# Performance work log

Measured on AMD Instinct MI355X. Metric: run time of the kernel, lower is better.

## Reference

```python
import jax, jax.numpy as jnp
import numpy as np

B, T, H, IN, OUT = 128, 256, 1024, 1, 1


def setup_inputs() -> dict:
    key = jax.random.key(0)
    ks = jax.random.split(key, 11)
    s = 1.0 / np.sqrt(H)
    u = lambda k, shape: jax.random.uniform(k, shape, jnp.float32, -s, s)
    return {
        "input_X": jax.random.normal(ks[0], (B, T), jnp.float32),
        "W_ih0": u(ks[1], (4 * H, IN)),
        "W_hh0": u(ks[2], (4 * H, H)),
        "b_ih0": u(ks[3], (4 * H,)),
        "b_hh0": u(ks[4], (4 * H,)),
        "W_ih1": u(ks[5], (4 * H, H)),
        "W_hh1": u(ks[6], (4 * H, H)),
        "b_ih1": u(ks[7], (4 * H,)),
        "b_hh1": u(ks[8], (4 * H,)),
        "W_lin": u(ks[9], (OUT, H)),
        "b_lin": u(ks[10], (OUT,)),
        "future": 0,
    }


def _lstm_cell(x, h, c, W_ih, W_hh, b_ih, b_hh):
    # gates: [B, 4H], PyTorch LSTMCell gate order: i, f, g, o
    gates = x @ W_ih.T + b_ih + h @ W_hh.T + b_hh
    i, f, g, o = jnp.split(gates, 4, axis=-1)
    c_new = jax.nn.sigmoid(f) * c + jax.nn.sigmoid(i) * jnp.tanh(g)
    h_new = jax.nn.sigmoid(o) * jnp.tanh(c_new)
    return h_new, c_new


def reference(input_X, W_ih0, W_hh0, b_ih0, b_hh0, W_ih1, W_hh1, b_ih1, b_hh1,
              W_lin, b_lin, future):
    batch = input_X.shape[0]
    h0 = jnp.zeros((batch, H), input_X.dtype)
    c0 = jnp.zeros((batch, H), input_X.dtype)
    h1 = jnp.zeros((batch, H), input_X.dtype)
    c1 = jnp.zeros((batch, H), input_X.dtype)

    def step(carry, x_t):  # x_t: [B, 1]
        h0, c0, h1, c1 = carry
        h0, c0 = _lstm_cell(x_t, h0, c0, W_ih0, W_hh0, b_ih0, b_hh0)
        h1, c1 = _lstm_cell(h0, h1, c1, W_ih1, W_hh1, b_ih1, b_hh1)
        y = h1 @ W_lin.T + b_lin  # [B, OUT]
        return (h0, c0, h1, c1), y

    xs = input_X.T[:, :, None]  # [T, B, 1]
    carry, ys = jax.lax.scan(step, (h0, c0, h1, c1), xs)
    outputs = jnp.transpose(ys, (1, 0, 2))  # [B, T, OUT]

    y = ys[-1]
    fut = []
    for _ in range(int(future)):
        carry, y = step(carry, y)
        fut.append(y)
    if fut:
        outputs = jnp.concatenate([outputs, jnp.stack(fut, axis=1)], axis=1)
    return jnp.squeeze(outputs, axis=2)  # [B, T+future]
```

## Files before the change

kernel.cpp:

```cpp
#include <hip/hip_runtime.h>
#include <stdint.h>

typedef _Float16 f16;
typedef f16 half8 __attribute__((ext_vector_type(8)));
typedef float f32x4 __attribute__((ext_vector_type(4)));

#define AS1 __attribute__((address_space(1)))
#define AS3 __attribute__((address_space(3)))

constexpr int HID = 1024;
constexpr int NBAT = 128;
constexpr int SEQ = 256;
constexpr int NL0 = 64;
constexpr int NL1 = 128;
constexpr int NBLK = NL0 + NL1;
constexpr int HROWB = 4096;
constexpr int WROWB0 = 2064;
constexpr int WROWB1 = 4112;
constexpr int ZOFF = 32 * WROWB1;
constexpr int ZBYTES = 4160;
constexpr int WLDS = ZOFF + ZBYTES;
constexpr int CHB = 8192;
constexpr int LDS_TOTAL = WLDS + 3 * CHB;

constexpr int SY_INIT = 0;
constexpr int SY_BARG = 32;
constexpr int SY_CNT = 64;
constexpr int SY_BARAX = 64 + 256;
constexpr int SY_TOTAL = 64 + 256 + 256;

__device__ __forceinline__ float sigm(float x) { return 1.0f / (1.0f + __expf(-x)); }
__device__ __forceinline__ float tanh_(float x) {
  float e = __expf(2.0f * x);
  return (e - 1.0f) / (e + 1.0f);
}
__device__ __forceinline__ void gl_lds16(const void* g, void* l) {
  __builtin_amdgcn_global_load_lds((const AS1 uint32_t*)g, (AS3 uint32_t*)l, 16, 0, 0);
}
__device__ __forceinline__ void vm0() {
  asm volatile("s_waitcnt vmcnt(0)" ::: "memory");
}
__device__ __forceinline__ void spin_until(int* p, int target) {
  uint64_t t0 = __builtin_amdgcn_s_memtime();
  while (__hip_atomic_load(p, __ATOMIC_RELAXED, __HIP_MEMORY_SCOPE_AGENT) < target) {
    __builtin_amdgcn_s_sleep(1);
    if (__builtin_amdgcn_s_memtime() - t0 > (1ULL << 29)) break;
  }
}

__global__ __launch_bounds__(256, 1) void lstm_persist(
    const float* __restrict__ X,
    const float* __restrict__ Wih0, const float* __restrict__ Whh0,
    const float* __restrict__ bih0, const float* __restrict__ bhh0,
    const float* __restrict__ Wih1, const float* __restrict__ Whh1,
    const float* __restrict__ bih1, const float* __restrict__ bhh1,
    const float* __restrict__ Wlin,
    f16* __restrict__ Hcat,
    float* __restrict__ yp,
    int* __restrict__ sy) {
  extern __shared__ char smem[];
  char* Wl = smem;
  char* Ach = smem + WLDS;

  const int bid = blockIdx.x, tid = threadIdx.x;
  const bool isL0 = bid < NL0;
  const int j = isL0 ? bid : bid - NL0;
  const int w = tid >> 6, l = tid & 63;
  const int l15 = l & 15, lhi = l >> 4;

  int xcd;
  asm volatile("s_getreg_b32 %0, hwreg(HW_REG_XCC_ID)" : "=s"(xcd));
  xcd &= 7;

  if (isL0) {
    for (int it = 0; it < 256; ++it) {
      int e = it * 256 + tid;
      int r = e >> 10, k = e & 1023;
      int grow = (r >> 4) * HID + j * 16 + (r & 15);
      *(f16*)(Wl + r * WROWB0 + 2 * k) = (f16)Whh0[(size_t)grow * HID + k];
    }
  } else {
    for (int it = 0; it < 256; ++it) {
      int e = it * 256 + tid;
      int r = e >> 11, k = e & 2047;
      int grow = (r >> 3) * HID + j * 8 + (r & 7);
      float v = (k < 1024) ? Wih1[(size_t)grow * HID + k]
                           : Whh1[(size_t)grow * HID + (k - 1024)];
      *(f16*)(Wl + r * WROWB1 + 2 * k) = (f16)v;
    }
    for (int e = tid; e < ZBYTES / 2; e += 256)
      *(f16*)(Wl + ZOFF + 2 * e) = (f16)0.f;
  }

  float bi, bf, bg, bo, wi_i = 0, wi_f = 0, wi_g = 0, wi_o = 0, wl = 0;
  if (isL0) {
    int m = j * 16 + l15;
    bi = bih0[m] + bhh0[m];
    bf = bih0[HID + m] + bhh0[HID + m];
    bg = bih0[2 * HID + m] + bhh0[2 * HID + m];
    bo = bih0[3 * HID + m] + bhh0[3 * HID + m];
    wi_i = Wih0[m]; wi_f = Wih0[HID + m];
    wi_g = Wih0[2 * HID + m]; wi_o = Wih0[3 * HID + m];
  } else {
    int u = j * 8 + (l15 & 7);
    bi = bih1[u] + bhh1[u];
    bf = bih1[HID + u] + bhh1[HID + u];
    bg = bih1[2 * HID + u] + bhh1[2 * HID + u];
    bo = bih1[3 * HID + u] + bhh1[3 * HID + u];
    wl = (l15 < 8) ? Wlin[u] : 0.f;
  }
  float cst[8];
#pragma unroll
  for (int q = 0; q < 8; ++q) cst[q] = 0.f;

  int cx = 0, nx = 0;
  if (tid == 0) {
    __hip_atomic_fetch_add(&sy[SY_CNT + 32 * xcd], 1, __ATOMIC_RELAXED,
                           __HIP_MEMORY_SCOPE_AGENT);
    __hip_atomic_fetch_add(&sy[SY_INIT], 1, __ATOMIC_RELAXED, __HIP_MEMORY_SCOPE_AGENT);
    spin_until(&sy[SY_INIT], NBLK);
    cx = __hip_atomic_load(&sy[SY_CNT + 32 * xcd], __ATOMIC_RELAXED,
                           __HIP_MEMORY_SCOPE_AGENT);
#pragma unroll
    for (int x = 0; x < 8; ++x)
      nx += (__hip_atomic_load(&sy[SY_CNT + 32 * x], __ATOMIC_RELAXED,
                               __HIP_MEMORY_SCOPE_AGENT) > 0);
  }
  __syncthreads();

  const char* Wb = Wl + l15 * WROWB0 + lhi * 16;
  const char* Wg0 = Wl + ((l15 < 8) ? (0 * 8 + l15) * WROWB1 : ZOFF) + lhi * 16;
  const char* Wg1 = Wl + ((l15 < 8) ? (1 * 8 + l15) * WROWB1 : ZOFF) + lhi * 16;
  const char* Wg2 = Wl + ((l15 < 8) ? (2 * 8 + l15) * WROWB1 : ZOFF) + lhi * 16;
  const char* Wg3 = Wl + ((l15 < 8) ? (3 * 8 + l15) * WROWB1 : ZOFF) + lhi * 16;

  const char* Ab = Ach + w * 2048 + (lhi * 32 + l15) * 16;
  char* dbase = Ach + w * 2048;

#define ISSUE(ck, buf)                                        \
  gl_lds16(arow + (ck) * 64, dbase + (buf) * CHB);            \
  gl_lds16(arow + (ck) * 64 + 32, dbase + (buf) * CHB + 1024);

  for (int i = 1; i <= SEQ + 1; ++i) {
    const bool active = isL0 ? (i <= SEQ) : (i >= 2);
    if (active) {
      const char* Asrc = (const char*)Hcat + (size_t)((i - 1) & 1) * NBAT * HROWB;
      const char* arow = Asrc + (size_t)(32 * w + (l & 31)) * HROWB + (l >> 5) * 16;
      f16* Hw = Hcat + (size_t)(i & 1) * NBAT * 2048;

      if (isL0) {
        float xr[8];
#pragma unroll
        for (int mf = 0; mf < 2; ++mf)
#pragma unroll
          for (int r = 0; r < 4; ++r)
            xr[mf * 4 + r] = X[(32 * w + 16 * mf + 4 * lhi + r) * SEQ + (i - 1)];
        vm0();
        __builtin_amdgcn_sched_barrier(0);

        ISSUE(0, 0) ISSUE(1, 1) ISSUE(2, 2)
        f32x4 acc[2][4];
#pragma unroll
        for (int mf = 0; mf < 2; ++mf)
#pragma unroll
          for (int n = 0; n < 4; ++n) acc[mf][n] = f32x4{0.f, 0.f, 0.f, 0.f};

        for (int ck = 0; ck < 32; ++ck) {
          if (ck <= 29) { asm volatile("s_waitcnt vmcnt(4)" ::: "memory"); }
          else if (ck == 30) { asm volatile("s_waitcnt vmcnt(2)" ::: "memory"); }
          else { asm volatile("s_waitcnt vmcnt(0)" ::: "memory"); }
          __builtin_amdgcn_sched_barrier(0);
          const int buf = ck % 3;
          half8 a0 = *(const half8*)(Ab + buf * CHB);
          half8 a1 = *(const half8*)(Ab + buf * CHB + 256);
          half8 b0 = *(const half8*)(Wb + ck * 64);
          half8 b1 = *(const half8*)(Wb + 16 * WROWB0 + ck * 64);
          half8 b2 = *(const half8*)(Wb + 32 * WROWB0 + ck * 64);
          half8 b3 = *(const half8*)(Wb + 48 * WROWB0 + ck * 64);
          asm volatile("s_waitcnt lgkmcnt(0)" ::: "memory");
          __builtin_amdgcn_sched_barrier(0);
          if (ck < 29) { ISSUE(ck + 3, buf) }
          acc[0][0] = __builtin_amdgcn_mfma_f32_16x16x32_f16(a0, b0, acc[0][0], 0, 0, 0);
          acc[0][1] = __builtin_amdgcn_mfma_f32_16x16x32_f16(a0, b1, acc[0][1], 0, 0, 0);
          acc[0][2] = __builtin_amdgcn_mfma_f32_16x16x32_f16(a0, b2, acc[0][2], 0, 0, 0);
          acc[0][3] = __builtin_amdgcn_mfma_f32_16x16x32_f16(a0, b3, acc[0][3], 0, 0, 0);
          acc[1][0] = __builtin_amdgcn_mfma_f32_16x16x32_f16(a1, b0, acc[1][0], 0, 0, 0);
          acc[1][1] = __builtin_amdgcn_mfma_f32_16x16x32_f16(a1, b1, acc[1][1], 0, 0, 0);
          acc[1][2] = __builtin_amdgcn_mfma_f32_16x16x32_f16(a1, b2, acc[1][2], 0, 0, 0);
          acc[1][3] = __builtin_amdgcn_mfma_f32_16x16x32_f16(a1, b3, acc[1][3], 0, 0, 0);
        }

#pragma unroll
        for (int mf = 0; mf < 2; ++mf) {
#pragma unroll
          for (int r = 0; r < 4; ++r) {
            int b = 32 * w + 16 * mf + 4 * lhi + r;
            float xv = xr[mf * 4 + r];
            float gi = acc[mf][0][r] + bi + xv * wi_i;
            float gf = acc[mf][1][r] + bf + xv * wi_f;
            float gg = acc[mf][2][r] + bg + xv * wi_g;
            float go = acc[mf][3][r] + bo + xv * wi_o;
            float cn = sigm(gf) * cst[mf * 4 + r] + sigm(gi) * tanh_(gg);
            float hn = sigm(go) * tanh_(cn);
            cst[mf * 4 + r] = cn;
            Hw[(size_t)b * 2048 + j * 16 + l15] = (f16)hn;
          }
        }
      } else {
        ISSUE(0, 0) ISSUE(1, 1) ISSUE(2, 2)
        f32x4 acc[2][4];
#pragma unroll
        for (int mf = 0; mf < 2; ++mf)
#pragma unroll
          for (int n = 0; n < 4; ++n) acc[mf][n] = f32x4{0.f, 0.f, 0.f, 0.f};

        for (int ck = 0; ck < 64; ++ck) {
          if (ck <= 61) { asm volatile("s_waitcnt vmcnt(4)" ::: "memory"); }
          else if (ck == 62) { asm volatile("s_waitcnt vmcnt(2)" ::: "memory"); }
          else { asm volatile("s_waitcnt vmcnt(0)" ::: "memory"); }
          __builtin_amdgcn_sched_barrier(0);
          const int buf = ck % 3;
          half8 a0 = *(const half8*)(Ab + buf * CHB);
          half8 a1 = *(const half8*)(Ab + buf * CHB + 256);
          half8 b0 = *(const half8*)(Wg0 + ck * 64);
          half8 b1 = *(const half8*)(Wg1 + ck * 64);
          half8 b2 = *(const half8*)(Wg2 + ck * 64);
          half8 b3 = *(const half8*)(Wg3 + ck * 64);
          asm volatile("s_waitcnt lgkmcnt(0)" ::: "memory");
          __builtin_amdgcn_sched_barrier(0);
          if (ck < 61) { ISSUE(ck + 3, buf) }
          acc[0][0] = __builtin_amdgcn_mfma_f32_16x16x32_f16(a0, b0, acc[0][0], 0, 0, 0);
          acc[0][1] = __builtin_amdgcn_mfma_f32_16x16x32_f16(a0, b1, acc[0][1], 0, 0, 0);
          acc[0][2] = __builtin_amdgcn_mfma_f32_16x16x32_f16(a0, b2, acc[0][2], 0, 0, 0);
          acc[0][3] = __builtin_amdgcn_mfma_f32_16x16x32_f16(a0, b3, acc[0][3], 0, 0, 0);
          acc[1][0] = __builtin_amdgcn_mfma_f32_16x16x32_f16(a1, b0, acc[1][0], 0, 0, 0);
          acc[1][1] = __builtin_amdgcn_mfma_f32_16x16x32_f16(a1, b1, acc[1][1], 0, 0, 0);
          acc[1][2] = __builtin_amdgcn_mfma_f32_16x16x32_f16(a1, b2, acc[1][2], 0, 0, 0);
          acc[1][3] = __builtin_amdgcn_mfma_f32_16x16x32_f16(a1, b3, acc[1][3], 0, 0, 0);
        }

#pragma unroll
        for (int mf = 0; mf < 2; ++mf) {
#pragma unroll
          for (int r = 0; r < 4; ++r) {
            int b = 32 * w + 16 * mf + 4 * lhi + r;
            float gi = acc[mf][0][r] + bi;
            float gf = acc[mf][1][r] + bf;
            float gg = acc[mf][2][r] + bg;
            float go = acc[mf][3][r] + bo;
            float cn = sigm(gf) * cst[mf * 4 + r] + sigm(gi) * tanh_(gg);
            float hn = sigm(go) * tanh_(cn);
            cst[mf * 4 + r] = cn;
            if (l15 < 8) Hw[(size_t)b * 2048 + 1024 + j * 8 + l15] = (f16)hn;
            float v = hn * wl;
            v += __shfl_xor(v, 1);
            v += __shfl_xor(v, 2);
            v += __shfl_xor(v, 4);
            v += __shfl_xor(v, 8);
            if (l15 == 0)
              yp[(size_t)(i - 2) * NBAT * NL1 + b * NL1 + j] = v;
          }
        }
      }
    }

    if (i <= SEQ) {
      vm0();
      __syncthreads();
      if (tid == 0) {
        int old = __hip_atomic_fetch_add(&sy[SY_BARAX + 32 * xcd], 1, __ATOMIC_RELAXED,
                                         __HIP_MEMORY_SCOPE_AGENT);
        if (old == cx * i - 1) {
          asm volatile("buffer_wbl2 sc1\n\ts_waitcnt vmcnt(0)" ::: "memory");
          asm volatile("buffer_inv sc1\n\ts_waitcnt vmcnt(0)" ::: "memory");
          __hip_atomic_fetch_add(&sy[SY_BARG], 1, __ATOMIC_RELAXED,
                                 __HIP_MEMORY_SCOPE_AGENT);
        }
        asm volatile("buffer_inv\n\ts_waitcnt vmcnt(0)" ::: "memory");
        spin_until(&sy[SY_BARG], nx * i);
      }
      __syncthreads();
    }
  }
#undef ISSUE
}

__global__ __launch_bounds__(256) void zero_ws(f16* Hcat, int* sy) {
  int g = blockIdx.x * 256 + threadIdx.x, gs = gridDim.x * 256;
  for (int idx = g; idx < 2 * NBAT * 2048; idx += gs) Hcat[idx] = (f16)0.f;
  for (int idx = g; idx < 1024; idx += gs) sy[idx] = 0;
}

__global__ __launch_bounds__(256) void final_kernel(const float* __restrict__ yp,
                                                    const float* __restrict__ blin,
                                                    float* __restrict__ out) {
  const int idx = blockIdx.x * blockDim.x + threadIdx.x;
  const int t = idx >> 7, b = idx & 127;
  const float* p = yp + ((size_t)t * NBAT + b) * NL1;
  float s = 0.f;
#pragma unroll
  for (int q = 0; q < NL1; ++q) s += p[q];
  out[b * SEQ + t] = s + blin[0];
}

extern "C" void kernel_launch(void* const* d_in, const int* in_sizes, int n_in,
                              void* d_out, int out_size, void* d_ws, size_t ws_size,
                              hipStream_t stream) {
  const float* X = (const float*)d_in[0];
  const float* Wih0 = (const float*)d_in[1];
  const float* Whh0 = (const float*)d_in[2];
  const float* bih0 = (const float*)d_in[3];
  const float* bhh0 = (const float*)d_in[4];
  const float* Wih1 = (const float*)d_in[5];
  const float* Whh1 = (const float*)d_in[6];
  const float* bih1 = (const float*)d_in[7];
  const float* bhh1 = (const float*)d_in[8];
  const float* Wlin = (const float*)d_in[9];
  const float* blin = (const float*)d_in[10];
  float* out = (float*)d_out;

  char* p = (char*)d_ws;
  f16* Hcat = (f16*)p;    p += (size_t)2 * NBAT * 2048 * 2;
  float* yp = (float*)p;  p += (size_t)SEQ * NBAT * NL1 * 4;
  int* sy = (int*)p;      p += 1024 * 4;

  hipFuncSetAttribute((const void*)lstm_persist,
                      hipFuncAttributeMaxDynamicSharedMemorySize, LDS_TOTAL);

  zero_ws<<<256, 256, 0, stream>>>(Hcat, sy);

  lstm_persist<<<NBLK, 256, LDS_TOTAL, stream>>>(
      X, Wih0, Whh0, bih0, bhh0, Wih1, Whh1, bih1, bhh1, Wlin,
      Hcat, yp, sy);

  final_kernel<<<NBAT, 256, 0, stream>>>(yp, blin, out);
}
```

Before: 5.209 ms.

## Load hidden-state A fragments directly into registers with 8-deep prefetch instead of LDS staging

Result: no change. 5.138 ms (-1.4%).

```diff
diff --git a/kernel.cpp b/kernel.cpp
--- a/kernel.cpp
+++ b/kernel.cpp
@@ -4,9 +4,6 @@
 typedef _Float16 f16;
 typedef f16 half8 __attribute__((ext_vector_type(8)));
 typedef float f32x4 __attribute__((ext_vector_type(4)));
-
-#define AS1 __attribute__((address_space(1)))
-#define AS3 __attribute__((address_space(3)))
 
 constexpr int HID = 1024;
 constexpr int NBAT = 128;
@@ -20,22 +17,17 @@
 constexpr int ZOFF = 32 * WROWB1;
 constexpr int ZBYTES = 4160;
 constexpr int WLDS = ZOFF + ZBYTES;
-constexpr int CHB = 8192;
-constexpr int LDS_TOTAL = WLDS + 3 * CHB;
+constexpr int LDS_TOTAL = WLDS;
 
 constexpr int SY_INIT = 0;
 constexpr int SY_BARG = 32;
 constexpr int SY_CNT = 64;
 constexpr int SY_BARAX = 64 + 256;
-constexpr int SY_TOTAL = 64 + 256 + 256;
 
 __device__ __forceinline__ float sigm(float x) { return 1.0f / (1.0f + __expf(-x)); }
 __device__ __forceinline__ float tanh_(float x) {
   float e = __expf(2.0f * x);
   return (e - 1.0f) / (e + 1.0f);
-}
-__device__ __forceinline__ void gl_lds16(const void* g, void* l) {
-  __builtin_amdgcn_global_load_lds((const AS1 uint32_t*)g, (AS3 uint32_t*)l, 16, 0, 0);
 }
 __device__ __forceinline__ void vm0() {
   asm volatile("s_waitcnt vmcnt(0)" ::: "memory");
@@ -60,7 +52,6 @@
     int* __restrict__ sy) {
   extern __shared__ char smem[];
   char* Wl = smem;
-  char* Ach = smem + WLDS;
 
   const int bid = blockIdx.x, tid = threadIdx.x;
   const bool isL0 = bid < NL0;
@@ -134,18 +125,12 @@
   const char* Wg2 = Wl + ((l15 < 8) ? (2 * 8 + l15) * WROWB1 : ZOFF) + lhi * 16;
   const char* Wg3 = Wl + ((l15 < 8) ? (3 * 8 + l15) * WROWB1 : ZOFF) + lhi * 16;
 
-  const char* Ab = Ach + w * 2048 + (lhi * 32 + l15) * 16;
-  char* dbase = Ach + w * 2048;
-
-#define ISSUE(ck, buf)                                        \
-  gl_lds16(arow + (ck) * 64, dbase + (buf) * CHB);            \
-  gl_lds16(arow + (ck) * 64 + 32, dbase + (buf) * CHB + 1024);
-
   for (int i = 1; i <= SEQ + 1; ++i) {
     const bool active = isL0 ? (i <= SEQ) : (i >= 2);
     if (active) {
       const char* Asrc = (const char*)Hcat + (size_t)((i - 1) & 1) * NBAT * HROWB;
-      const char* arow = Asrc + (size_t)(32 * w + (l & 31)) * HROWB + (l >> 5) * 16;
+      const char* a0p = Asrc + (size_t)(32 * w + l15) * HROWB + lhi * 16;
+      const char* a1p = a0p + (size_t)16 * HROWB;
       f16* Hw = Hcat + (size_t)(i & 1) * NBAT * 2048;
 
       if (isL0) {
@@ -155,31 +140,30 @@
 #pragma unroll
           for (int r = 0; r < 4; ++r)
             xr[mf * 4 + r] = X[(32 * w + 16 * mf + 4 * lhi + r) * SEQ + (i - 1)];
-        vm0();
-        __builtin_amdgcn_sched_barrier(0);
-
-        ISSUE(0, 0) ISSUE(1, 1) ISSUE(2, 2)
+
+        half8 pa[8], pb[8];
+#pragma unroll
+        for (int k0 = 0; k0 < 8; ++k0) {
+          pa[k0] = *(const half8*)(a0p + k0 * 64);
+          pb[k0] = *(const half8*)(a1p + k0 * 64);
+        }
         f32x4 acc[2][4];
 #pragma unroll
         for (int mf = 0; mf < 2; ++mf)
 #pragma unroll
           for (int n = 0; n < 4; ++n) acc[mf][n] = f32x4{0.f, 0.f, 0.f, 0.f};
 
+#pragma unroll
         for (int ck = 0; ck < 32; ++ck) {
-          if (ck <= 29) { asm volatile("s_waitcnt vmcnt(4)" ::: "memory"); }
-          else if (ck == 30) { asm volatile("s_waitcnt vmcnt(2)" ::: "memory"); }
-          else { asm volatile("s_waitcnt vmcnt(0)" ::: "memory"); }
-          __builtin_amdgcn_sched_barrier(0);
-          const int buf = ck % 3;
-          half8 a0 = *(const half8*)(Ab + buf * CHB);
-          half8 a1 = *(const half8*)(Ab + buf * CHB + 256);
+          half8 a0 = pa[ck & 7], a1 = pb[ck & 7];
+          if (ck < 24) {
+            pa[ck & 7] = *(const half8*)(a0p + (ck + 8) * 64);
+            pb[ck & 7] = *(const half8*)(a1p + (ck + 8) * 64);
+          }
           half8 b0 = *(const half8*)(Wb + ck * 64);
           half8 b1 = *(const half8*)(Wb + 16 * WROWB0 + ck * 64);
           half8 b2 = *(const half8*)(Wb + 32 * WROWB0 + ck * 64);
           half8 b3 = *(const half8*)(Wb + 48 * WROWB0 + ck * 64);
-          asm volatile("s_waitcnt lgkmcnt(0)" ::: "memory");
-          __builtin_amdgcn_sched_barrier(0);
-          if (ck < 29) { ISSUE(ck + 3, buf) }
           acc[0][0] = __builtin_amdgcn_mfma_f32_16x16x32_f16(a0, b0, acc[0][0], 0, 0, 0);
           acc[0][1] = __builtin_amdgcn_mfma_f32_16x16x32_f16(a0, b1, acc[0][1], 0, 0, 0);
           acc[0][2] = __builtin_amdgcn_mfma_f32_16x16x32_f16(a0, b2, acc[0][2], 0, 0, 0);
@@ -207,28 +191,29 @@
           }
         }
       } else {
-        ISSUE(0, 0) ISSUE(1, 1) ISSUE(2, 2)
+        half8 pa[8], pb[8];
+#pragma unroll
+        for (int k0 = 0; k0 < 8; ++k0) {
+          pa[k0] = *(const half8*)(a0p + k0 * 64);
+          pb[k0] = *(const half8*)(a1p + k0 * 64);
+        }
         f32x4 acc[2][4];
 #pragma unroll
         for (int mf = 0; mf < 2; ++mf)
 #pragma unroll
           for (int n = 0; n < 4; ++n) acc[mf][n] = f32x4{0.f, 0.f, 0.f, 0.f};
 
+#pragma unroll
         for (int ck = 0; ck < 64; ++ck) {
-          if (ck <= 61) { asm volatile("s_waitcnt vmcnt(4)" ::: "memory"); }
-          else if (ck == 62) { asm volatile("s_waitcnt vmcnt(2)" ::: "memory"); }
-          else { asm volatile("s_waitcnt vmcnt(0)" ::: "memory"); }
-          __builtin_amdgcn_sched_barrier(0);
-          const int buf = ck % 3;
-          half8 a0 = *(const half8*)(Ab + buf * CHB);
-          half8 a1 = *(const half8*)(Ab + buf * CHB + 256);
+          half8 a0 = pa[ck & 7], a1 = pb[ck & 7];
+          if (ck < 56) {
+            pa[ck & 7] = *(const half8*)(a0p + (ck + 8) * 64);
+            pb[ck & 7] = *(const half8*)(a1p + (ck + 8) * 64);
+          }
           half8 b0 = *(const half8*)(Wg0 + ck * 64);
           half8 b1 = *(const half8*)(Wg1 + ck * 64);
           half8 b2 = *(const half8*)(Wg2 + ck * 64);
           half8 b3 = *(const half8*)(Wg3 + ck * 64);
-          asm volatile("s_waitcnt lgkmcnt(0)" ::: "memory");
-          __builtin_amdgcn_sched_barrier(0);
-          if (ck < 61) { ISSUE(ck + 3, buf) }
           acc[0][0] = __builtin_amdgcn_mfma_f32_16x16x32_f16(a0, b0, acc[0][0], 0, 0, 0);
           acc[0][1] = __builtin_amdgcn_mfma_f32_16x16x32_f16(a0, b1, acc[0][1], 0, 0, 0);
           acc[0][2] = __builtin_amdgcn_mfma_f32_16x16x32_f16(a0, b2, acc[0][2], 0, 0, 0);
@@ -282,7 +267,6 @@
       __syncthreads();
     }
   }
-#undef ISSUE
 }
 
 __global__ __launch_bounds__(256) void zero_ws(f16* Hcat, int* sy) {
```
